# Optimization experiments

Measured on AMD Instinct MI355X. Metric: run time of the kernel, lower is better.

Reference implementation:

```python
import jax, jax.numpy as jnp
import numpy as np

N, E, F_IN, H, O = 50000, 800000, 128, 8, 8  # nodes, edges, in_feat, heads, out-per-head
NEG_SLOPE = 0.2

def setup_inputs() -> dict:
    key = jax.random.key(0)
    k1, k2, k3, k4, k5, k6 = jax.random.split(key, 6)
    h = jax.random.normal(k1, (N, F_IN), dtype=jnp.float32)
    # xavier_uniform-like scale (gain=1.414) expressed via normal init scale
    w_scale = 1.414 * np.sqrt(2.0 / (F_IN + O)).astype(np.float32)
    W = jax.random.normal(k2, (H, F_IN, O), dtype=jnp.float32) * w_scale
    a_scale = 1.414 * np.sqrt(2.0 / (2 * O + 1)).astype(np.float32)
    a1 = jax.random.normal(k3, (H, O), dtype=jnp.float32) * a_scale
    a2 = jax.random.normal(k4, (H, O), dtype=jnp.float32) * a_scale
    src = jax.random.randint(k5, (E,), 0, N, dtype=jnp.int64 if jax.config.jax_enable_x64 else jnp.int32)
    dst = jax.random.randint(k6, (E,), 0, N, dtype=jnp.int64 if jax.config.jax_enable_x64 else jnp.int32)
    return {"h": h, "W": W, "a1": a1, "a2": a2, "src": src, "dst": dst}

def reference(h, W, a1, a2, src, dst):
    # Per-head linear projection: [N, H, O]
    Wh = jnp.einsum('nf,hfo->nho', h, W)
    # Per-node attention half-scores (a split into src/dst halves): [N, H]
    s_src = jnp.einsum('nho,ho->nh', Wh, a1)
    s_dst = jnp.einsum('nho,ho->nh', Wh, a2)
    # Edge attention logits: [E, H]
    e = jax.nn.leaky_relu(s_src[src] + s_dst[dst], negative_slope=NEG_SLOPE)
    # Numerically-stable segment softmax over incoming edges of each dst node
    m = jax.ops.segment_max(e, dst, num_segments=N)          # [N, H]
    m = jnp.where(jnp.isfinite(m), m, jnp.float32(0.0))      # isolated nodes -> 0
    p = jnp.exp(e - m[dst])                                   # [E, H]
    denom = jax.ops.segment_sum(p, dst, num_segments=N)       # [N, H]
    attn = p / jnp.maximum(denom[dst], jnp.float32(1e-16))    # [E, H]
    # Weighted scatter-sum of messages: [N, H, O]
    out = jax.ops.segment_sum(attn[:, :, None] * Wh[src], dst, num_segments=N)
    # Concatenate heads: [N, H*O]
    return out.reshape(N, H * O)
```

## Files before the change

kernel.cpp:

```cpp
#include <hip/hip_runtime.h>
#include <hip/hip_bf16.h>
#include <hip/hip_fp16.h>


#define FIN 128
#define NH 8
#define NO 8
#define NC 64
#define NB_COLS 80
#define GR 64
#define EPB 4096
#define BCAP 8192

typedef __attribute__((ext_vector_type(8))) short bf16x8;
typedef __attribute__((ext_vector_type(4))) float f32x4;

static __device__ __forceinline__ unsigned short f2bf(float f) {
    unsigned u = __float_as_uint(f);
    u += 0x7fff + ((u >> 16) & 1);
    return (unsigned short)(u >> 16);
}

__global__ __launch_bounds__(256) void prep_kernel(
    const float* __restrict__ W, const float* __restrict__ a1, const float* __restrict__ a2,
    unsigned short* __restrict__ wBg, int* __restrict__ bcnt)
{
    const int t = threadIdx.x;
    bcnt[t] = 0;
    for (int i = t; i < NH * FIN * NO; i += 256) {
        int hh = i >> 10, f = (i >> 3) & 127, o = i & 7;
        int c = hh * 8 + o;
        wBg[c * FIN + (f ^ ((c & 7) << 3))] = f2bf(W[i]);
    }
    for (int i = t; i < 16 * FIN; i += 256) {
        int j = i >> 7;
        int f = i & 127;
        int hh = j & 7;
        const float* av = (j < 8) ? (a1 + hh * NO) : (a2 + hh * NO);
        const float* wv = W + hh * (FIN * NO) + f * NO;
        float s = 0.f;
#pragma unroll
        for (int o = 0; o < 8; ++o) s += wv[o] * av[o];
        int c = 64 + j;
        wBg[c * FIN + (f ^ ((c & 7) << 3))] = f2bf(s);
    }
}

__global__ __launch_bounds__(256) void gemm_s_scat_kernel(
    const float* __restrict__ h, const unsigned short* __restrict__ wBg,
    const int* __restrict__ src, const int* __restrict__ dst,
    int* __restrict__ bcnt, unsigned* __restrict__ packed,
    __half* __restrict__ Wh, float* __restrict__ s_src, float* __restrict__ s_dst,
    int N, int E, int gemm_blocks)
{
    __shared__ alignas(16) unsigned short wB[NB_COLS * FIN];
    __shared__ int cnt_l[256];
    __shared__ int base_l[256];
    const int tid = threadIdx.x;

    if (blockIdx.x >= gemm_blocks) {
        const long e0 = (long)(blockIdx.x - gemm_blocks) * EPB;
        cnt_l[tid] = 0;
        __syncthreads();
        int br[16];
        unsigned pk[16];
#pragma unroll
        for (int j = 0; j < 16; ++j) {
            long e = e0 + j * 256 + tid;
            bool ok = (e < E);
            int d = ok ? dst[e] : 0;
            int s = ok ? src[e] : 0;
            int b = d >> 8;
            int r = ok ? atomicAdd(&cnt_l[b], 1) : 0;
            br[j] = ok ? ((b << 16) | r) : -1;
            pk[j] = ((unsigned)(d & 255) << 16) | (unsigned)s;
        }
        __syncthreads();
        if (cnt_l[tid] > 0) base_l[tid] = atomicAdd(&bcnt[tid], cnt_l[tid]);
        __syncthreads();
#pragma unroll
        for (int j = 0; j < 16; ++j) {
            if (br[j] >= 0) {
                int b = br[j] >> 16, r = br[j] & 0xFFFF;
                packed[(long)b * BCAP + base_l[b] + r] = pk[j];
            }
        }
        return;
    }

    const int w    = tid >> 6;
    const int lane = tid & 63;
    const int l15  = lane & 15;
    const int lg   = lane >> 4;

    const int row  = blockIdx.x * GR + w * 16 + l15;
    const int rowc = (row < N) ? row : (N - 1);
    const float* hrow = h + (long)rowc * FIN + lg * 8;
    float4 va[8];
#pragma unroll
    for (int kk = 0; kk < 4; ++kk) {
        va[2 * kk]     = *(const float4*)(hrow + kk * 32);
        va[2 * kk + 1] = *(const float4*)(hrow + kk * 32 + 4);
    }

    {
        const uint4* s4 = (const uint4*)wBg;
        uint4* d4 = (uint4*)wB;
#pragma unroll
        for (int j = 0; j < 5; ++j)
            d4[j * 256 + tid] = s4[j * 256 + tid];
    }
    __syncthreads();

    bf16x8 af[4];
#pragma unroll
    for (int kk = 0; kk < 4; ++kk) {
        bf16x8 r;
        r[0] = (short)f2bf(va[2 * kk].x);     r[1] = (short)f2bf(va[2 * kk].y);
        r[2] = (short)f2bf(va[2 * kk].z);     r[3] = (short)f2bf(va[2 * kk].w);
        r[4] = (short)f2bf(va[2 * kk + 1].x); r[5] = (short)f2bf(va[2 * kk + 1].y);
        r[6] = (short)f2bf(va[2 * kk + 1].z); r[7] = (short)f2bf(va[2 * kk + 1].w);
        af[kk] = r;
    }

    f32x4 acc[5] = {{0,0,0,0},{0,0,0,0},{0,0,0,0},{0,0,0,0},{0,0,0,0}};
#pragma unroll
    for (int kk = 0; kk < 4; ++kk) {
        int kb = kk * 64 + lg * 16;
#pragma unroll
        for (int nt = 0; nt < 5; ++nt) {
            int c = nt * 16 + l15;
            bf16x8 bf = *(const bf16x8*)((const char*)wB + c * (FIN * 2) + (kb ^ ((c & 7) << 4)));
            acc[nt] = __builtin_amdgcn_mfma_f32_16x16x32_bf16(af[kk], bf, acc[nt], 0, 0, 0);
        }
    }

    const int row0 = blockIdx.x * GR;
#pragma unroll
    for (int nt = 0; nt < 4; ++nt) {
        int col = nt * 16 + l15;
#pragma unroll
        for (int r = 0; r < 4; ++r) {
            int n = row0 + w * 16 + lg * 4 + r;
            if (n < N) Wh[(long)n * NC + col] = __float2half_rn(acc[nt][r]);
        }
    }
#pragma unroll
    for (int r = 0; r < 4; ++r) {
        int n = row0 + w * 16 + lg * 4 + r;
        if (n < N) {
            float v = acc[4][r];
            if (l15 < 8) s_src[n * NH + l15] = v;
            else         s_dst[n * NH + (l15 - 8)] = v;
        }
    }
}

__global__ __launch_bounds__(1024) void bucketB_kernel(
    const unsigned* __restrict__ packed, const int* __restrict__ bcnt,
    int* __restrict__ row_off, unsigned short* __restrict__ srcs,
    int N, int E, int nb)
{
    __shared__ int bins[256];
    __shared__ int scan_s[256];
    __shared__ int g0s;
    __shared__ unsigned short outb[BCAP];
    const int t = threadIdx.x;
    const int b = blockIdx.x;
    const int d0 = b << 8;
    const unsigned* pin = packed + (long)b * BCAP;

    int v2 = 0;
    if (t < 256) {
        v2 = (t < nb) ? bcnt[t] : 0;
        scan_s[t] = v2;
        bins[t] = 0;
    }
    __syncthreads();
    for (int off = 1; off < 256; off <<= 1) {
        int u = (t < 256 && t >= off) ? scan_s[t - off] : 0;
        __syncthreads();
        if (t < 256) scan_s[t] += u;
        __syncthreads();
    }
    if (t == b) g0s = scan_s[t] - v2;
    __syncthreads();
    const int g0 = g0s;
    const int cnt = bcnt[b];

    for (int i = t; i < cnt; i += 1024)
        atomicAdd(&bins[pin[i] >> 16], 1);
    __syncthreads();
    int v = 0;
    if (t < 256) { v = bins[t]; scan_s[t] = v; }
    __syncthreads();
    for (int off = 1; off < 256; off <<= 1) {
        int u = (t < 256 && t >= off) ? scan_s[t - off] : 0;
        __syncthreads();
        if (t < 256) scan_s[t] += u;
        __syncthreads();
    }
    if (t < 256) {
        if (d0 + t < N) row_off[d0 + t] = g0 + scan_s[t] - v;
        bins[t] = scan_s[t] - v;
    }
    if (b == nb - 1 && t == 0) row_off[N] = E;
    __syncthreads();
    for (int i = t; i < cnt; i += 1024) {
        unsigned p = pin[i];
        int pos = atomicAdd(&bins[p >> 16], 1);
        outb[pos] = (unsigned short)(p & 0xFFFF);
    }
    __syncthreads();
    for (int i = t; i < cnt; i += 1024)
        srcs[g0 + i] = outb[i];
}

__global__ __launch_bounds__(256) void gather_kernel(
    const unsigned short* __restrict__ srcs, const int* __restrict__ row_off,
    const float* __restrict__ s_src, const float* __restrict__ s_dst,
    const __half* __restrict__ Wh, float* __restrict__ out, int N)
{
    const int w    = threadIdx.x >> 6;
    const int lane = threadIdx.x & 63;
    const int half = lane >> 5;
    const int hb   = half << 5;
    const int ll   = lane & 31;
    const int el   = ll >> 3;
    const int hh   = ll & 7;
    const int q    = ll >> 2;
    const int node = blockIdx.x * 8 + w * 2 + half;
    const bool nvalid = (node < N);

    int beg = nvalid ? row_off[node] : 0;
    int end = nvalid ? row_off[node + 1] : 0;
    float sd = nvalid ? s_dst[node * NH + hh] : 0.f;
    float acc0 = 0.f, acc1 = 0.f, den = 0.f;

    int idx0 = beg + el;
    bool val = (idx0 < end);
    int s = (int)srcs[val ? idx0 : beg];
    float ss = s_src[s * NH + hh];

    const unsigned* Wh32 = (const unsigned*)Wh;
    for (int i = beg; i < end; i += 4) {
        int nidx = i + 4 + el;
        bool nval = (nidx < end);
        int ns = (int)srcs[nval ? nidx : beg];
        float nss = s_src[ns * NH + hh];
        float x = ss + sd;
        x = (x > 0.f) ? x : 0.2f * x;
        float p = __expf(x);
        p = val ? p : 0.f;
        den += p;
#pragma unroll
        for (int k = 0; k < 4; ++k) {
            int sk   = __shfl(s, hb + k * 8);
            float pk = __shfl(p, hb + k * 8 + q);
            unsigned wu = Wh32[((unsigned)sk << 5) + ll];
            float2 wf = __half22float2(*(__half2*)&wu);
            acc0 = fmaf(pk, wf.x, acc0);
            acc1 = fmaf(pk, wf.y, acc1);
        }
        s = ns; ss = nss; val = nval;
    }
    den += __shfl_xor(den, 8);
    den += __shfl_xor(den, 16);
    float den_b = __shfl(den, hb + q);
    if (nvalid) {
        float r = 1.f / fmaxf(den_b, 1e-16f);
        float2 o; o.x = acc0 * r; o.y = acc1 * r;
        ((float2*)out)[((unsigned)node << 5) + ll] = o;
    }
}

extern "C" void kernel_launch(void* const* d_in, const int* in_sizes, int n_in,
                              void* d_out, int out_size, void* d_ws, size_t ws_size,
                              hipStream_t stream)
{
    const float* h  = (const float*)d_in[0];
    const float* W  = (const float*)d_in[1];
    const float* a1 = (const float*)d_in[2];
    const float* a2 = (const float*)d_in[3];
    const int*  src = (const int*)d_in[4];
    const int*  dst = (const int*)d_in[5];
    float* out = (float*)d_out;

    const int N = in_sizes[0] / FIN;
    const int E = in_sizes[4];
    const int nb = (N + 255) >> 8;

    char* wsb = (char*)d_ws;
    __half* Wh         = (__half*)wsb;           wsb += (size_t)N * NC * 2;
    float* s_src       = (float*)wsb;            wsb += (size_t)N * NH * 4;
    float* s_dst       = (float*)wsb;            wsb += (size_t)N * NH * 4;
    int* row_off       = (int*)wsb;              wsb += (size_t)(N + 1) * 4;
    int* bcnt          = (int*)wsb;              wsb += (size_t)256 * 4;
    unsigned short* wBg = (unsigned short*)wsb;  wsb += (size_t)NB_COLS * FIN * 2;
    unsigned* packed   = (unsigned*)wsb;         wsb += (size_t)nb * BCAP * 4;
    unsigned short* srcs = (unsigned short*)wsb; wsb += (size_t)E * 2;

    prep_kernel<<<1, 256, 0, stream>>>(W, a1, a2, wBg, bcnt);

    const int gemm_blocks = (N + GR - 1) / GR;
    const int scat_blocks = (E + EPB - 1) / EPB;
    gemm_s_scat_kernel<<<gemm_blocks + scat_blocks, 256, 0, stream>>>(
        h, wBg, src, dst, bcnt, packed, Wh, s_src, s_dst, N, E, gemm_blocks);

    bucketB_kernel<<<nb, 1024, 0, stream>>>(packed, bcnt, row_off, srcs, N, E, nb);

    int g_blocks = (N + 7) / 8;
    gather_kernel<<<g_blocks, 256, 0, stream>>>(srcs, row_off, s_src, s_dst, Wh, out, N);
}
```

Before: 62.13 us.

## Process two row tiles per GEMM block and schedule scatter blocks first

Each GEMM block now handles 128 rows instead of 64, with every wave computing two 16-row tiles that share each B-fragment LDS read, so the per-block copy of the weight matrix into shared memory is amortized over twice as many rows. The fused launch is reordered so the edge-scatter blocks get the low block indices and are dispatched before the GEMM blocks. This halves the GEMM block count at the cost of more registers per thread, which may reduce occupancy, and fewer blocks to spread across CUs.

```diff
diff --git a/kernel.cpp b/kernel.cpp
--- a/kernel.cpp
+++ b/kernel.cpp
@@ -8,7 +8,7 @@
 #define NO 8
 #define NC 64
 #define NB_COLS 80
-#define GR 64
+#define GR 128
 #define EPB 4096
 #define BCAP 8192
 
@@ -51,15 +51,15 @@
     const int* __restrict__ src, const int* __restrict__ dst,
     int* __restrict__ bcnt, unsigned* __restrict__ packed,
     __half* __restrict__ Wh, float* __restrict__ s_src, float* __restrict__ s_dst,
-    int N, int E, int gemm_blocks)
+    int N, int E, int scat_blocks)
 {
     __shared__ alignas(16) unsigned short wB[NB_COLS * FIN];
     __shared__ int cnt_l[256];
     __shared__ int base_l[256];
     const int tid = threadIdx.x;
 
-    if (blockIdx.x >= gemm_blocks) {
-        const long e0 = (long)(blockIdx.x - gemm_blocks) * EPB;
+    if (blockIdx.x < scat_blocks) {
+        const long e0 = (long)blockIdx.x * EPB;
         cnt_l[tid] = 0;
         __syncthreads();
         int br[16];
@@ -92,15 +92,21 @@
     const int lane = tid & 63;
     const int l15  = lane & 15;
     const int lg   = lane >> 4;
-
-    const int row  = blockIdx.x * GR + w * 16 + l15;
-    const int rowc = (row < N) ? row : (N - 1);
-    const float* hrow = h + (long)rowc * FIN + lg * 8;
-    float4 va[8];
+    const int row0 = (blockIdx.x - scat_blocks) * GR;
+
+    const int rowA = row0 + w * 16 + l15;
+    const int rowB = rowA + 64;
+    const int rcA = (rowA < N) ? rowA : (N - 1);
+    const int rcB = (rowB < N) ? rowB : (N - 1);
+    const float* hrowA = h + (long)rcA * FIN + lg * 8;
+    const float* hrowB = h + (long)rcB * FIN + lg * 8;
+    float4 va[8], vb[8];
 #pragma unroll
     for (int kk = 0; kk < 4; ++kk) {
-        va[2 * kk]     = *(const float4*)(hrow + kk * 32);
-        va[2 * kk + 1] = *(const float4*)(hrow + kk * 32 + 4);
+        va[2 * kk]     = *(const float4*)(hrowA + kk * 32);
+        va[2 * kk + 1] = *(const float4*)(hrowA + kk * 32 + 4);
+        vb[2 * kk]     = *(const float4*)(hrowB + kk * 32);
+        vb[2 * kk + 1] = *(const float4*)(hrowB + kk * 32 + 4);
     }
 
     {
@@ -112,46 +118,57 @@
     }
     __syncthreads();
 
-    bf16x8 af[4];
+    bf16x8 af[4], bf_[4];
 #pragma unroll
     for (int kk = 0; kk < 4; ++kk) {
-        bf16x8 r;
+        bf16x8 r, r2;
         r[0] = (short)f2bf(va[2 * kk].x);     r[1] = (short)f2bf(va[2 * kk].y);
         r[2] = (short)f2bf(va[2 * kk].z);     r[3] = (short)f2bf(va[2 * kk].w);
         r[4] = (short)f2bf(va[2 * kk + 1].x); r[5] = (short)f2bf(va[2 * kk + 1].y);
         r[6] = (short)f2bf(va[2 * kk + 1].z); r[7] = (short)f2bf(va[2 * kk + 1].w);
         af[kk] = r;
-    }
-
-    f32x4 acc[5] = {{0,0,0,0},{0,0,0,0},{0,0,0,0},{0,0,0,0},{0,0,0,0}};
+        r2[0] = (short)f2bf(vb[2 * kk].x);     r2[1] = (short)f2bf(vb[2 * kk].y);
+        r2[2] = (short)f2bf(vb[2 * kk].z);     r2[3] = (short)f2bf(vb[2 * kk].w);
+        r2[4] = (short)f2bf(vb[2 * kk + 1].x); r2[5] = (short)f2bf(vb[2 * kk + 1].y);
+        r2[6] = (short)f2bf(vb[2 * kk + 1].z); r2[7] = (short)f2bf(vb[2 * kk + 1].w);
+        bf_[kk] = r2;
+    }
+
+    f32x4 accA[5] = {{0,0,0,0},{0,0,0,0},{0,0,0,0},{0,0,0,0},{0,0,0,0}};
+    f32x4 accB[5] = {{0,0,0,0},{0,0,0,0},{0,0,0,0},{0,0,0,0},{0,0,0,0}};
 #pragma unroll
     for (int kk = 0; kk < 4; ++kk) {
         int kb = kk * 64 + lg * 16;
 #pragma unroll
         for (int nt = 0; nt < 5; ++nt) {
             int c = nt * 16 + l15;
-            bf16x8 bf = *(const bf16x8*)((const char*)wB + c * (FIN * 2) + (kb ^ ((c & 7) << 4)));
-            acc[nt] = __builtin_amdgcn_mfma_f32_16x16x32_bf16(af[kk], bf, acc[nt], 0, 0, 0);
-        }
-    }
-
-    const int row0 = blockIdx.x * GR;
-#pragma unroll
-    for (int nt = 0; nt < 4; ++nt) {
-        int col = nt * 16 + l15;
+            bf16x8 bfr = *(const bf16x8*)((const char*)wB + c * (FIN * 2) + (kb ^ ((c & 7) << 4)));
+            accA[nt] = __builtin_amdgcn_mfma_f32_16x16x32_bf16(af[kk], bfr, accA[nt], 0, 0, 0);
+            accB[nt] = __builtin_amdgcn_mfma_f32_16x16x32_bf16(bf_[kk], bfr, accB[nt], 0, 0, 0);
+        }
+    }
+
+#pragma unroll
+    for (int t2 = 0; t2 < 2; ++t2) {
+        const f32x4* acc = t2 ? accB : accA;
+        const int rbase = row0 + t2 * 64 + w * 16 + lg * 4;
+#pragma unroll
+        for (int nt = 0; nt < 4; ++nt) {
+            int col = nt * 16 + l15;
+#pragma unroll
+            for (int r = 0; r < 4; ++r) {
+                int n = rbase + r;
+                if (n < N) Wh[(long)n * NC + col] = __float2half_rn(acc[nt][r]);
+            }
+        }
 #pragma unroll
         for (int r = 0; r < 4; ++r) {
-            int n = row0 + w * 16 + lg * 4 + r;
-            if (n < N) Wh[(long)n * NC + col] = __float2half_rn(acc[nt][r]);
-        }
-    }
-#pragma unroll
-    for (int r = 0; r < 4; ++r) {
-        int n = row0 + w * 16 + lg * 4 + r;
-        if (n < N) {
-            float v = acc[4][r];
-            if (l15 < 8) s_src[n * NH + l15] = v;
-            else         s_dst[n * NH + (l15 - 8)] = v;
+            int n = rbase + r;
+            if (n < N) {
+                float v = acc[4][r];
+                if (l15 < 8) s_src[n * NH + l15] = v;
+                else         s_dst[n * NH + (l15 - 8)] = v;
+            }
         }
     }
 }
@@ -304,8 +321,8 @@
 
     const int gemm_blocks = (N + GR - 1) / GR;
     const int scat_blocks = (E + EPB - 1) / EPB;
-    gemm_s_scat_kernel<<<gemm_blocks + scat_blocks, 256, 0, stream>>>(
-        h, wBg, src, dst, bcnt, packed, Wh, s_src, s_dst, N, E, gemm_blocks);
+    gemm_s_scat_kernel<<<scat_blocks + gemm_blocks, 256, 0, stream>>>(
+        h, wBg, src, dst, bcnt, packed, Wh, s_src, s_dst, N, E, scat_blocks);
 
     bucketB_kernel<<<nb, 1024, 0, stream>>>(packed, bcnt, row_off, srcs, N, E, nb);
 
```

Result: no change. 61.30 us, median of 3 (-1.3%).

## Fuse prep, scatter, GEMM and bucketing into one cooperative persistent kernel

Applied to the files above, without the earlier changes.

Replaces the three front kernels (weight prep, GEMM plus edge scatter, per-bucket sort) with one cooperative persistent kernel. Phases are separated by grid.sync, and the GEMM tiles and bucket sorts share the last phase through a unit loop. The aim is to cut kernel launch gaps and let the bucket sort overlap with GEMM work. The bucket phase now uses 256 threads instead of 1024, and grid-wide barriers add their own cost.

```diff
diff --git a/kernel.cpp b/kernel.cpp
--- a/kernel.cpp
+++ b/kernel.cpp
@@ -1,6 +1,9 @@
 #include <hip/hip_runtime.h>
 #include <hip/hip_bf16.h>
 #include <hip/hip_fp16.h>
+#include <hip/hip_cooperative_groups.h>
+
+namespace cg = cooperative_groups;
 
 
 #define FIN 128
@@ -21,199 +24,197 @@
     return (unsigned short)(u >> 16);
 }
 
-__global__ __launch_bounds__(256) void prep_kernel(
-    const float* __restrict__ W, const float* __restrict__ a1, const float* __restrict__ a2,
-    unsigned short* __restrict__ wBg, int* __restrict__ bcnt)
-{
-    const int t = threadIdx.x;
-    bcnt[t] = 0;
-    for (int i = t; i < NH * FIN * NO; i += 256) {
-        int hh = i >> 10, f = (i >> 3) & 127, o = i & 7;
-        int c = hh * 8 + o;
-        wBg[c * FIN + (f ^ ((c & 7) << 3))] = f2bf(W[i]);
-    }
-    for (int i = t; i < 16 * FIN; i += 256) {
-        int j = i >> 7;
-        int f = i & 127;
-        int hh = j & 7;
-        const float* av = (j < 8) ? (a1 + hh * NO) : (a2 + hh * NO);
-        const float* wv = W + hh * (FIN * NO) + f * NO;
-        float s = 0.f;
-#pragma unroll
-        for (int o = 0; o < 8; ++o) s += wv[o] * av[o];
-        int c = 64 + j;
-        wBg[c * FIN + (f ^ ((c & 7) << 3))] = f2bf(s);
-    }
-}
-
-__global__ __launch_bounds__(256) void gemm_s_scat_kernel(
-    const float* __restrict__ h, const unsigned short* __restrict__ wBg,
+__global__ __launch_bounds__(256, 4) void fused_front_kernel(
+    const float* __restrict__ h, const float* __restrict__ W,
+    const float* __restrict__ a1, const float* __restrict__ a2,
     const int* __restrict__ src, const int* __restrict__ dst,
     int* __restrict__ bcnt, unsigned* __restrict__ packed,
+    unsigned short* __restrict__ wBg,
     __half* __restrict__ Wh, float* __restrict__ s_src, float* __restrict__ s_dst,
-    int N, int E, int gemm_blocks)
+    int* __restrict__ row_off, unsigned short* __restrict__ srcs,
+    int N, int E, int scat_units, int gemm_units, int nb)
 {
-    __shared__ alignas(16) unsigned short wB[NB_COLS * FIN];
-    __shared__ int cnt_l[256];
-    __shared__ int base_l[256];
+    cg::grid_group grid = cg::this_grid();
+    __shared__ alignas(16) unsigned char smem[NB_COLS * FIN * 2];
+    __shared__ int g0s;
     const int tid = threadIdx.x;
 
-    if (blockIdx.x >= gemm_blocks) {
-        const long e0 = (long)(blockIdx.x - gemm_blocks) * EPB;
-        cnt_l[tid] = 0;
+    {
+        int g = blockIdx.x * 256 + tid;
+        int stride = gridDim.x * 256;
+        if (g < 256) bcnt[g] = 0;
+        for (int i = g; i < NH * FIN * NO; i += stride) {
+            int hh = i >> 10, f = (i >> 3) & 127, o = i & 7;
+            int c = hh * 8 + o;
+            wBg[c * FIN + (f ^ ((c & 7) << 3))] = f2bf(W[i]);
+        }
+        for (int i = g; i < 16 * FIN; i += stride) {
+            int j = i >> 7;
+            int f = i & 127;
+            int hh = j & 7;
+            const float* av = (j < 8) ? (a1 + hh * NO) : (a2 + hh * NO);
+            const float* wv = W + hh * (FIN * NO) + f * NO;
+            float s = 0.f;
+#pragma unroll
+            for (int o = 0; o < 8; ++o) s += wv[o] * av[o];
+            int c = 64 + j;
+            wBg[c * FIN + (f ^ ((c & 7) << 3))] = f2bf(s);
+        }
+    }
+    __threadfence();
+    grid.sync();
+
+    {
+        int* cnt_l  = (int*)smem;
+        int* base_l = (int*)(smem + 1024);
+        for (int u = blockIdx.x; u < scat_units; u += gridDim.x) {
+            const long e0 = (long)u * EPB;
+            cnt_l[tid] = 0;
+            __syncthreads();
+            int br[16];
+            unsigned pk[16];
+#pragma unroll
+            for (int j = 0; j < 16; ++j) {
+                long e = e0 + j * 256 + tid;
+                bool ok = (e < E);
+                int d = ok ? dst[e] : 0;
+                int s = ok ? src[e] : 0;
+                int b = d >> 8;
+                int r = ok ? atomicAdd(&cnt_l[b], 1) : 0;
+                br[j] = ok ? ((b << 16) | r) : -1;
+                pk[j] = ((unsigned)(d & 255) << 16) | (unsigned)s;
+            }
+            __syncthreads();
+            if (cnt_l[tid] > 0) base_l[tid] = atomicAdd(&bcnt[tid], cnt_l[tid]);
+            __syncthreads();
+#pragma unroll
+            for (int j = 0; j < 16; ++j) {
+                if (br[j] >= 0) {
+                    int b = br[j] >> 16, r = br[j] & 0xFFFF;
+                    packed[(long)b * BCAP + base_l[b] + r] = pk[j];
+                }
+            }
+            __syncthreads();
+        }
+    }
+    __threadfence();
+    grid.sync();
+
+    const int total2 = gemm_units + nb;
+    for (int u = blockIdx.x; u < total2; u += gridDim.x) {
+        if (u < gemm_units) {
+            unsigned short* wB = (unsigned short*)smem;
+            const int w    = tid >> 6;
+            const int lane = tid & 63;
+            const int l15  = lane & 15;
+            const int lg   = lane >> 4;
+            const int row0 = u * GR;
+            const int row  = row0 + w * 16 + l15;
+            const int rowc = (row < N) ? row : (N - 1);
+            const float* hrow = h + (long)rowc * FIN + lg * 8;
+            float4 va[8];
+#pragma unroll
+            for (int kk = 0; kk < 4; ++kk) {
+                va[2 * kk]     = *(const float4*)(hrow + kk * 32);
+                va[2 * kk + 1] = *(const float4*)(hrow + kk * 32 + 4);
+            }
+            {
+                const uint4* s4 = (const uint4*)wBg;
+                uint4* d4 = (uint4*)wB;
+#pragma unroll
+                for (int j = 0; j < 5; ++j)
+                    d4[j * 256 + tid] = s4[j * 256 + tid];
+            }
+            __syncthreads();
+            bf16x8 af[4];
+#pragma unroll
+            for (int kk = 0; kk < 4; ++kk) {
+                bf16x8 r;
+                r[0] = (short)f2bf(va[2 * kk].x);     r[1] = (short)f2bf(va[2 * kk].y);
+                r[2] = (short)f2bf(va[2 * kk].z);     r[3] = (short)f2bf(va[2 * kk].w);
+                r[4] = (short)f2bf(va[2 * kk + 1].x); r[5] = (short)f2bf(va[2 * kk + 1].y);
+                r[6] = (short)f2bf(va[2 * kk + 1].z); r[7] = (short)f2bf(va[2 * kk + 1].w);
+                af[kk] = r;
+            }
+            f32x4 acc[5] = {{0,0,0,0},{0,0,0,0},{0,0,0,0},{0,0,0,0},{0,0,0,0}};
+#pragma unroll
+            for (int kk = 0; kk < 4; ++kk) {
+                int kb = kk * 64 + lg * 16;
+#pragma unroll
+                for (int nt = 0; nt < 5; ++nt) {
+                    int c = nt * 16 + l15;
+                    bf16x8 bfr = *(const bf16x8*)((const char*)wB + c * (FIN * 2) + (kb ^ ((c & 7) << 4)));
+                    acc[nt] = __builtin_amdgcn_mfma_f32_16x16x32_bf16(af[kk], bfr, acc[nt], 0, 0, 0);
+                }
+            }
+#pragma unroll
+            for (int nt = 0; nt < 4; ++nt) {
+                int col = nt * 16 + l15;
+#pragma unroll
+                for (int r = 0; r < 4; ++r) {
+                    int n = row0 + w * 16 + lg * 4 + r;
+                    if (n < N) Wh[(long)n * NC + col] = __float2half_rn(acc[nt][r]);
+                }
+            }
+#pragma unroll
+            for (int r = 0; r < 4; ++r) {
+                int n = row0 + w * 16 + lg * 4 + r;
+                if (n < N) {
+                    float v = acc[4][r];
+                    if (l15 < 8) s_src[n * NH + l15] = v;
+                    else         s_dst[n * NH + (l15 - 8)] = v;
+                }
+            }
+        } else {
+            int* bins   = (int*)smem;
+            int* scan_s = (int*)(smem + 1024);
+            unsigned short* outb = (unsigned short*)(smem + 2048);
+            const int b = u - gemm_units;
+            const int d0 = b << 8;
+            const unsigned* pin = packed + (long)b * BCAP;
+
+            int v2 = (tid < nb) ? bcnt[tid] : 0;
+            scan_s[tid] = v2;
+            __syncthreads();
+            for (int off = 1; off < 256; off <<= 1) {
+                int uu = (tid >= off) ? scan_s[tid - off] : 0;
+                __syncthreads();
+                scan_s[tid] += uu;
+                __syncthreads();
+            }
+            if (tid == b) g0s = scan_s[tid] - v2;
+            bins[tid] = 0;
+            __syncthreads();
+            const int g0 = g0s;
+            const int cnt = bcnt[b];
+
+            for (int i = tid; i < cnt; i += 256)
+                atomicAdd(&bins[pin[i] >> 16], 1);
+            __syncthreads();
+            int v = bins[tid];
+            scan_s[tid] = v;
+            __syncthreads();
+            for (int off = 1; off < 256; off <<= 1) {
+                int uu = (tid >= off) ? scan_s[tid - off] : 0;
+                __syncthreads();
+                scan_s[tid] += uu;
+                __syncthreads();
+            }
+            if (d0 + tid < N) row_off[d0 + tid] = g0 + scan_s[tid] - v;
+            if (b == nb - 1 && tid == 0) row_off[N] = E;
+            bins[tid] = scan_s[tid] - v;
+            __syncthreads();
+            for (int i = tid; i < cnt; i += 256) {
+                unsigned p = pin[i];
+                int pos = atomicAdd(&bins[p >> 16], 1);
+                outb[pos] = (unsigned short)(p & 0xFFFF);
+            }
+            __syncthreads();
+            for (int i = tid; i < cnt; i += 256)
+                srcs[g0 + i] = outb[i];
+        }
         __syncthreads();
-        int br[16];
-        unsigned pk[16];
-#pragma unroll
-        for (int j = 0; j < 16; ++j) {
-            long e = e0 + j * 256 + tid;
-            bool ok = (e < E);
-            int d = ok ? dst[e] : 0;
-            int s = ok ? src[e] : 0;
-            int b = d >> 8;
-            int r = ok ? atomicAdd(&cnt_l[b], 1) : 0;
-            br[j] = ok ? ((b << 16) | r) : -1;
-            pk[j] = ((unsigned)(d & 255) << 16) | (unsigned)s;
-        }
-        __syncthreads();
-        if (cnt_l[tid] > 0) base_l[tid] = atomicAdd(&bcnt[tid], cnt_l[tid]);
-        __syncthreads();
-#pragma unroll
-        for (int j = 0; j < 16; ++j) {
-            if (br[j] >= 0) {
-                int b = br[j] >> 16, r = br[j] & 0xFFFF;
-                packed[(long)b * BCAP + base_l[b] + r] = pk[j];
-            }
-        }
-        return;
-    }
-
-    const int w    = tid >> 6;
-    const int lane = tid & 63;
-    const int l15  = lane & 15;
-    const int lg   = lane >> 4;
-
-    const int row  = blockIdx.x * GR + w * 16 + l15;
-    const int rowc = (row < N) ? row : (N - 1);
-    const float* hrow = h + (long)rowc * FIN + lg * 8;
-    float4 va[8];
-#pragma unroll
-    for (int kk = 0; kk < 4; ++kk) {
-        va[2 * kk]     = *(const float4*)(hrow + kk * 32);
-        va[2 * kk + 1] = *(const float4*)(hrow + kk * 32 + 4);
-    }
-
-    {
-        const uint4* s4 = (const uint4*)wBg;
-        uint4* d4 = (uint4*)wB;
-#pragma unroll
-        for (int j = 0; j < 5; ++j)
-            d4[j * 256 + tid] = s4[j * 256 + tid];
-    }
-    __syncthreads();
-
-    bf16x8 af[4];
-#pragma unroll
-    for (int kk = 0; kk < 4; ++kk) {
-        bf16x8 r;
-        r[0] = (short)f2bf(va[2 * kk].x);     r[1] = (short)f2bf(va[2 * kk].y);
-        r[2] = (short)f2bf(va[2 * kk].z);     r[3] = (short)f2bf(va[2 * kk].w);
-        r[4] = (short)f2bf(va[2 * kk + 1].x); r[5] = (short)f2bf(va[2 * kk + 1].y);
-        r[6] = (short)f2bf(va[2 * kk + 1].z); r[7] = (short)f2bf(va[2 * kk + 1].w);
-        af[kk] = r;
-    }
-
-    f32x4 acc[5] = {{0,0,0,0},{0,0,0,0},{0,0,0,0},{0,0,0,0},{0,0,0,0}};
-#pragma unroll
-    for (int kk = 0; kk < 4; ++kk) {
-        int kb = kk * 64 + lg * 16;
-#pragma unroll
-        for (int nt = 0; nt < 5; ++nt) {
-            int c = nt * 16 + l15;
-            bf16x8 bf = *(const bf16x8*)((const char*)wB + c * (FIN * 2) + (kb ^ ((c & 7) << 4)));
-            acc[nt] = __builtin_amdgcn_mfma_f32_16x16x32_bf16(af[kk], bf, acc[nt], 0, 0, 0);
-        }
-    }
-
-    const int row0 = blockIdx.x * GR;
-#pragma unroll
-    for (int nt = 0; nt < 4; ++nt) {
-        int col = nt * 16 + l15;
-#pragma unroll
-        for (int r = 0; r < 4; ++r) {
-            int n = row0 + w * 16 + lg * 4 + r;
-            if (n < N) Wh[(long)n * NC + col] = __float2half_rn(acc[nt][r]);
-        }
-    }
-#pragma unroll
-    for (int r = 0; r < 4; ++r) {
-        int n = row0 + w * 16 + lg * 4 + r;
-        if (n < N) {
-            float v = acc[4][r];
-            if (l15 < 8) s_src[n * NH + l15] = v;
-            else         s_dst[n * NH + (l15 - 8)] = v;
-        }
-    }
-}
-
-__global__ __launch_bounds__(1024) void bucketB_kernel(
-    const unsigned* __restrict__ packed, const int* __restrict__ bcnt,
-    int* __restrict__ row_off, unsigned short* __restrict__ srcs,
-    int N, int E, int nb)
-{
-    __shared__ int bins[256];
-    __shared__ int scan_s[256];
-    __shared__ int g0s;
-    __shared__ unsigned short outb[BCAP];
-    const int t = threadIdx.x;
-    const int b = blockIdx.x;
-    const int d0 = b << 8;
-    const unsigned* pin = packed + (long)b * BCAP;
-
-    int v2 = 0;
-    if (t < 256) {
-        v2 = (t < nb) ? bcnt[t] : 0;
-        scan_s[t] = v2;
-        bins[t] = 0;
-    }
-    __syncthreads();
-    for (int off = 1; off < 256; off <<= 1) {
-        int u = (t < 256 && t >= off) ? scan_s[t - off] : 0;
-        __syncthreads();
-        if (t < 256) scan_s[t] += u;
-        __syncthreads();
-    }
-    if (t == b) g0s = scan_s[t] - v2;
-    __syncthreads();
-    const int g0 = g0s;
-    const int cnt = bcnt[b];
-
-    for (int i = t; i < cnt; i += 1024)
-        atomicAdd(&bins[pin[i] >> 16], 1);
-    __syncthreads();
-    int v = 0;
-    if (t < 256) { v = bins[t]; scan_s[t] = v; }
-    __syncthreads();
-    for (int off = 1; off < 256; off <<= 1) {
-        int u = (t < 256 && t >= off) ? scan_s[t - off] : 0;
-        __syncthreads();
-        if (t < 256) scan_s[t] += u;
-        __syncthreads();
-    }
-    if (t < 256) {
-        if (d0 + t < N) row_off[d0 + t] = g0 + scan_s[t] - v;
-        bins[t] = scan_s[t] - v;
-    }
-    if (b == nb - 1 && t == 0) row_off[N] = E;
-    __syncthreads();
-    for (int i = t; i < cnt; i += 1024) {
-        unsigned p = pin[i];
-        int pos = atomicAdd(&bins[p >> 16], 1);
-        outb[pos] = (unsigned short)(p & 0xFFFF);
-    }
-    __syncthreads();
-    for (int i = t; i < cnt; i += 1024)
-        srcs[g0 + i] = outb[i];
+    }
 }
 
 __global__ __launch_bounds__(256) void gather_kernel(
@@ -300,14 +301,24 @@
     unsigned* packed   = (unsigned*)wsb;         wsb += (size_t)nb * BCAP * 4;
     unsigned short* srcs = (unsigned short*)wsb; wsb += (size_t)E * 2;
 
-    prep_kernel<<<1, 256, 0, stream>>>(W, a1, a2, wBg, bcnt);
-
-    const int gemm_blocks = (N + GR - 1) / GR;
-    const int scat_blocks = (E + EPB - 1) / EPB;
-    gemm_s_scat_kernel<<<gemm_blocks + scat_blocks, 256, 0, stream>>>(
-        h, wBg, src, dst, bcnt, packed, Wh, s_src, s_dst, N, E, gemm_blocks);
-
-    bucketB_kernel<<<nb, 1024, 0, stream>>>(packed, bcnt, row_off, srcs, N, E, nb);
+    int scat_units = (E + EPB - 1) / EPB;
+    int gemm_units = (N + GR - 1) / GR;
+    int total2 = gemm_units + nb;
+
+    int bpc = 0;
+    hipOccupancyMaxActiveBlocksPerMultiprocessor(&bpc, fused_front_kernel, 256, 0);
+    if (bpc < 1) bpc = 1;
+    long cap = (long)bpc * 256;
+    int grid = (int)((cap < (long)total2) ? cap : (long)total2);
+
+    void* args[] = {
+        (void*)&h, (void*)&W, (void*)&a1, (void*)&a2, (void*)&src, (void*)&dst,
+        (void*)&bcnt, (void*)&packed, (void*)&wBg, (void*)&Wh, (void*)&s_src, (void*)&s_dst,
+        (void*)&row_off, (void*)&srcs,
+        (void*)&N, (void*)&E, (void*)&scat_units, (void*)&gemm_units, (void*)&nb
+    };
+    hipLaunchCooperativeKernel(reinterpret_cast<void*>(fused_front_kernel),
+                               dim3(grid), dim3(256), args, 0, stream);
 
     int g_blocks = (N + 7) / 8;
     gather_kernel<<<g_blocks, 256, 0, stream>>>(srcs, row_off, s_src, s_dst, Wh, out, N);
```

After: 227.1 us. 266% more time.
